# Optimization experiments

Measured on AMD Instinct MI355X. Metric: run time of the kernel, lower is better.

## Reference

```python
import jax, jax.numpy as jnp
import numpy as np
import math

C, N, D, D_CTX = 256, 512, 256, 256
K = 24
HOMEOSTASIS = 0.01
FEEDBACK = 0.3
B = 64


def setup_inputs() -> dict:
    key = jax.random.key(0)
    k1, k2, k3, k4, k5 = jax.random.split(key, 5)
    ff_scale = math.sqrt(2.0 / (D + N))
    ctx_scale = math.sqrt(2.0 / (D_CTX + N))
    pred_scale = math.sqrt(2.0 / (N + D))
    return {
        "x_input": jax.random.normal(k1, (B, D), dtype=jnp.float32),
        "x_context": jax.random.normal(k2, (B, D_CTX), dtype=jnp.float32),
        "W_ff": jax.random.normal(k3, (C, D, N), dtype=jnp.float32) * ff_scale,
        "W_ctx": jax.random.normal(k4, (C, D_CTX, N), dtype=jnp.float32) * ctx_scale,
        "W_pred": jax.random.normal(k5, (C, N, D), dtype=jnp.float32) * pred_scale,
        "bias": jnp.zeros((C, N), dtype=jnp.float32),
        "avg_activity": jnp.full((C, N), 0.05, dtype=jnp.float32),
    }


def _k_winners(drive, avg_activity, k):
    # homeostatic boosting: boost * homeostasis * 100
    boost = jnp.log1p(0.05 / (avg_activity + 1e-6))  # [C, N]
    boosted = drive + boost[None] * (HOMEOSTASIS * 100.0)
    topk_vals = jax.lax.top_k(boosted, k)[0]  # [B, C, k]
    threshold = jax.lax.stop_gradient(topk_vals[..., -1:])  # [B, C, 1]
    mask = (boosted >= threshold).astype(drive.dtype)
    activation = jax.nn.relu(drive) * mask
    activation = activation / (jnp.sum(activation, axis=-1, keepdims=True) + 1e-8) * k
    return activation


def reference(x_input, x_context, W_ff, W_ctx, W_pred, bias, avg_activity):
    # per-column feedforward + context drive: [B, C, N]
    ff_drive = jnp.einsum('bd,cdn->bcn', x_input, W_ff)
    ctx_drive = jnp.einsum('bd,cdn->bcn', x_context, W_ctx)
    drive = ff_drive + ctx_drive * FEEDBACK + bias[None]
    activations = _k_winners(drive, avg_activity, K)  # [B, C, N]
    predictions = jnp.einsum('bcn,cnd->bcd', activations, W_pred)  # [B, C, D]
    errors = x_input[:, None, :] - predictions  # [B, C, D]
    return activations, predictions, errors
```

## Files before the change

kernel.cpp:

```cpp
#include <hip/hip_runtime.h>
#include <math.h>

#define CC 256
#define NN 512
#define DD 256
#define BB 64
#define KK 24
#define WCAP 48

#define MAT_F (BB * NN)
#define SMEM_FLOATS (MAT_F + BB + BB + NN + BB + BB * WCAP * 2)
#define SMEM_BYTES (SMEM_FLOATS * 4)

__global__ void transpose_x_kernel(const float* __restrict__ x_in,
                                   const float* __restrict__ x_ctx,
                                   float* __restrict__ xT) {
  int idx = blockIdx.x * blockDim.x + threadIdx.x;
  int d = idx >> 6;
  int b = idx & 63;
  float v = (d < DD) ? x_in[b * DD + d] : 0.3f * x_ctx[b * DD + (d - DD)];
  xT[idx] = v;
}

__launch_bounds__(1024)
__global__ void cortical_main(const float* __restrict__ x_in,
                              const float* __restrict__ xT,
                              const float* __restrict__ W_ff,
                              const float* __restrict__ W_ctx,
                              const float* __restrict__ W_pred,
                              const float* __restrict__ bias,
                              const float* __restrict__ avg_act,
                              float* __restrict__ out_act,
                              float* __restrict__ out_pred,
                              float* __restrict__ out_err) {
  extern __shared__ float smem[];
  float* mat = smem;
  float* thr = smem + MAT_F;
  float* scl = thr + BB;
  float* boostS = scl + BB;
  int* wcnt = (int*)(boostS + NN);
  float* wlist = (float*)(wcnt + BB);

  const int c = blockIdx.x;
  const int t = threadIdx.x;
  const int lane = t & 63;
  const int wv = t >> 6;

  if (t < NN) boostS[t] = log1pf(0.05f / (avg_act[c * NN + t] + 1e-6f));
  __syncthreads();

  const int ng = t & 255;
  const int n0 = ng * 2;
  const int b0 = __builtin_amdgcn_readfirstlane((t >> 8) * 16);

  float acc[16][2];
#pragma unroll
  for (int i = 0; i < 16; ++i) { acc[i][0] = 0.f; acc[i][1] = 0.f; }

  const float* __restrict__ wf = W_ff + (size_t)c * DD * NN + n0;
  const float* __restrict__ wc = W_ctx + (size_t)c * DD * NN + n0;

#pragma unroll 4
  for (int d = 0; d < DD; ++d) {
    const float2 w = *reinterpret_cast<const float2*>(wf + (size_t)d * NN);
    const float* __restrict__ xp = xT + d * BB + b0;
#pragma unroll
    for (int i = 0; i < 16; ++i) {
      const float xv = xp[i];
      acc[i][0] = fmaf(xv, w.x, acc[i][0]);
      acc[i][1] = fmaf(xv, w.y, acc[i][1]);
    }
  }
#pragma unroll 4
  for (int d = 0; d < DD; ++d) {
    const float2 w = *reinterpret_cast<const float2*>(wc + (size_t)d * NN);
    const float* __restrict__ xp = xT + (DD + d) * BB + b0;
#pragma unroll
    for (int i = 0; i < 16; ++i) {
      const float xv = xp[i];
      acc[i][0] = fmaf(xv, w.x, acc[i][0]);
      acc[i][1] = fmaf(xv, w.y, acc[i][1]);
    }
  }

  const float2 bz = *reinterpret_cast<const float2*>(bias + (size_t)c * NN + n0);
  const float2 bo = *reinterpret_cast<const float2*>(boostS + n0);
#pragma unroll
  for (int i = 0; i < 16; ++i) {
    float d0v = acc[i][0] + bz.x;
    float d1v = acc[i][1] + bz.y;
    float2 m2;
    m2.x = d0v + bo.x;
    m2.y = d1v + bo.y;
    *reinterpret_cast<float2*>(mat + (size_t)(b0 + i) * NN + n0) = m2;
  }
  __syncthreads();

  for (int r = wv * 4; r < wv * 4 + 4; ++r) {
    float v[8];
#pragma unroll
    for (int j = 0; j < 8; ++j) v[j] = mat[r * NN + lane + 64 * j];
    float kth = 0.f;
    for (int it = 0; it < KK; ++it) {
      float m = v[0];
#pragma unroll
      for (int j = 1; j < 8; ++j) m = fmaxf(m, v[j]);
#pragma unroll
      for (int off = 1; off <= 32; off <<= 1) m = fmaxf(m, __shfl_xor(m, off));
      kth = m;
      bool mine = false;
#pragma unroll
      for (int j = 0; j < 8; ++j) mine = mine || (v[j] == m);
      unsigned long long msk = __ballot(mine);
      int first = __ffsll((unsigned long long)msk) - 1;
      if (lane == first) {
        bool done = false;
#pragma unroll
        for (int j = 0; j < 8; ++j) {
          bool cnd = (!done) && (v[j] == m);
          if (cnd) v[j] = -INFINITY;
          done = done || cnd;
        }
      }
    }
    if (lane == 0) thr[r] = kth;
  }
  __syncthreads();

  for (int r = wv * 4; r < wv * 4 + 4; ++r) {
    const float tb = thr[r];
    float raw[8];
    float s = 0.f;
#pragma unroll
    for (int j = 0; j < 8; ++j) {
      const int n = lane + 64 * j;
      const float bv = mat[r * NN + n];
      const float rw = (bv >= tb) ? fmaxf(bv - boostS[n], 0.f) : 0.f;
      raw[j] = rw;
      s += rw;
    }
#pragma unroll
    for (int off = 1; off <= 32; off <<= 1) s += __shfl_xor(s, off);
    const float sc = (float)KK / (s + 1e-8f);

    int base = 0;
#pragma unroll
    for (int j = 0; j < 8; ++j) {
      const int n = lane + 64 * j;
      const float a = raw[j] * sc;
      out_act[(size_t)r * (CC * NN) + (size_t)c * NN + n] = a;
      const bool win = a > 0.f;
      unsigned long long m = __ballot(win);
      int pos = base + __popcll(m & ((1ull << lane) - 1ull));
      if (win && pos < WCAP) {
        const int slot = (r * WCAP + pos) * 2;
        wlist[slot] = a;
        reinterpret_cast<int*>(wlist)[slot + 1] = n;
      }
      base += (int)__popcll(m);
    }
    if (lane == 0) wcnt[r] = (base < WCAP) ? base : WCAP;
  }
  __syncthreads();

  {
    const int dq = t & 63;
    const int d0 = dq * 4;
    const int grp = t >> 6;
    const float* __restrict__ wp = W_pred + (size_t)c * NN * DD;
    for (int bi = 0; bi < 4; ++bi) {
      const int b = grp * 4 + bi;
      const int cnt = wcnt[b];
      float4 p = make_float4(0.f, 0.f, 0.f, 0.f);
      float4 q = make_float4(0.f, 0.f, 0.f, 0.f);
      int i = 0;
      for (; i + 2 <= cnt; i += 2) {
        const int s0 = (b * WCAP + i) * 2;
        const int s1 = s0 + 2;
        const float a0 = wlist[s0];
        const int nn0 = reinterpret_cast<const int*>(wlist)[s0 + 1];
        const float a1 = wlist[s1];
        const int nn1 = reinterpret_cast<const int*>(wlist)[s1 + 1];
        const float4 w0 = *reinterpret_cast<const float4*>(wp + (size_t)nn0 * DD + d0);
        const float4 w1 = *reinterpret_cast<const float4*>(wp + (size_t)nn1 * DD + d0);
        p.x = fmaf(a0, w0.x, p.x); p.y = fmaf(a0, w0.y, p.y);
        p.z = fmaf(a0, w0.z, p.z); p.w = fmaf(a0, w0.w, p.w);
        q.x = fmaf(a1, w1.x, q.x); q.y = fmaf(a1, w1.y, q.y);
        q.z = fmaf(a1, w1.z, q.z); q.w = fmaf(a1, w1.w, q.w);
      }
      if (i < cnt) {
        const int s0 = (b * WCAP + i) * 2;
        const float a0 = wlist[s0];
        const int nn0 = reinterpret_cast<const int*>(wlist)[s0 + 1];
        const float4 w0 = *reinterpret_cast<const float4*>(wp + (size_t)nn0 * DD + d0);
        p.x = fmaf(a0, w0.x, p.x); p.y = fmaf(a0, w0.y, p.y);
        p.z = fmaf(a0, w0.z, p.z); p.w = fmaf(a0, w0.w, p.w);
      }
      float4 r4;
      r4.x = p.x + q.x; r4.y = p.y + q.y; r4.z = p.z + q.z; r4.w = p.w + q.w;
      const float4 xi = *reinterpret_cast<const float4*>(x_in + (size_t)b * DD + d0);
      float4 e4;
      e4.x = xi.x - r4.x; e4.y = xi.y - r4.y; e4.z = xi.z - r4.z; e4.w = xi.w - r4.w;
      *reinterpret_cast<float4*>(out_pred + (size_t)b * (CC * DD) + (size_t)c * DD + d0) = r4;
      *reinterpret_cast<float4*>(out_err + (size_t)b * (CC * DD) + (size_t)c * DD + d0) = e4;
    }
  }
}

extern "C" void kernel_launch(void* const* d_in, const int* in_sizes, int n_in,
                              void* d_out, int out_size, void* d_ws, size_t ws_size,
                              hipStream_t stream) {
  const float* x_in = (const float*)d_in[0];
  const float* x_ctx = (const float*)d_in[1];
  const float* W_ff = (const float*)d_in[2];
  const float* W_ctx = (const float*)d_in[3];
  const float* W_pred = (const float*)d_in[4];
  const float* bias = (const float*)d_in[5];
  const float* avg = (const float*)d_in[6];

  float* out = (float*)d_out;
  float* out_act = out;
  float* out_pred = out + (size_t)BB * CC * NN;
  float* out_err = out_pred + (size_t)BB * CC * DD;

  float* xT = (float*)d_ws;

  hipFuncSetAttribute((const void*)cortical_main,
                      hipFuncAttributeMaxDynamicSharedMemorySize, SMEM_BYTES);

  transpose_x_kernel<<<(2 * BB * DD) / 256, 256, 0, stream>>>(x_in, x_ctx, xT);
  cortical_main<<<CC, 1024, SMEM_BYTES, stream>>>(x_in, xT, W_ff, W_ctx, W_pred,
                                                  bias, avg, out_act, out_pred,
                                                  out_err);
}
```

Measured before the change: 218.9 us.

## Split fused kernel into drive GEMM and sparse top-k prediction kernels

Splits the single per-column kernel into a drive GEMM launched on twice as many blocks (each block covers half of N), writing the boosted drive to a workspace buffer, and a second kernel that reads it, does top-k, and computes the sparse prediction. The aim is to raise occupancy, since the old kernel needed about 140KB of LDS per block, and to remove the shared-memory staging and some barriers. In exchange it adds an extra global round trip of 32MB of drive data. The old fused kernel is kept as a fallback for when the workspace is too small.

Result: slower. 230.8 us (+5.4%).

```diff
diff --git a/kernel.cpp b/kernel.cpp
--- a/kernel.cpp
+++ b/kernel.cpp
@@ -7,10 +7,6 @@
 #define BB 64
 #define KK 24
 #define WCAP 48
-
-#define MAT_F (BB * NN)
-#define SMEM_FLOATS (MAT_F + BB + BB + NN + BB + BB * WCAP * 2)
-#define SMEM_BYTES (SMEM_FLOATS * 4)
 
 __global__ void transpose_x_kernel(const float* __restrict__ x_in,
                                    const float* __restrict__ x_ctx,
@@ -22,84 +18,92 @@
   xT[idx] = v;
 }
 
+__launch_bounds__(512)
+__global__ void drive_gemm(const float* __restrict__ xT,
+                           const float* __restrict__ W_ff,
+                           const float* __restrict__ W_ctx,
+                           const float* __restrict__ bias,
+                           const float* __restrict__ avg_act,
+                           float* __restrict__ driveB) {
+  const int c = blockIdx.x >> 1;
+  const int nh = blockIdx.x & 1;
+  const int t = threadIdx.x;
+  const int ng = t & 127;
+  const int n0 = nh * 256 + ng * 2;
+  const int b0 = __builtin_amdgcn_readfirstlane((t >> 7) * 16);
+
+  float2 acc[16];
+#pragma unroll
+  for (int i = 0; i < 16; ++i) { acc[i].x = 0.f; acc[i].y = 0.f; }
+
+  const float* __restrict__ wf = W_ff + (size_t)c * DD * NN + n0;
+  const float* __restrict__ wc = W_ctx + (size_t)c * DD * NN + n0;
+
+#pragma unroll 4
+  for (int d = 0; d < DD; ++d) {
+    const float2 w = *reinterpret_cast<const float2*>(wf + (size_t)d * NN);
+    const float* __restrict__ xp = xT + d * BB + b0;
+#pragma unroll
+    for (int i = 0; i < 16; ++i) {
+      const float xv = xp[i];
+      acc[i].x = fmaf(xv, w.x, acc[i].x);
+      acc[i].y = fmaf(xv, w.y, acc[i].y);
+    }
+  }
+#pragma unroll 4
+  for (int d = 0; d < DD; ++d) {
+    const float2 w = *reinterpret_cast<const float2*>(wc + (size_t)d * NN);
+    const float* __restrict__ xp = xT + (DD + d) * BB + b0;
+#pragma unroll
+    for (int i = 0; i < 16; ++i) {
+      const float xv = xp[i];
+      acc[i].x = fmaf(xv, w.x, acc[i].x);
+      acc[i].y = fmaf(xv, w.y, acc[i].y);
+    }
+  }
+
+  const float2 bz = *reinterpret_cast<const float2*>(bias + (size_t)c * NN + n0);
+  const float2 av = *reinterpret_cast<const float2*>(avg_act + (size_t)c * NN + n0);
+  float2 bo;
+  bo.x = log1pf(0.05f / (av.x + 1e-6f));
+  bo.y = log1pf(0.05f / (av.y + 1e-6f));
+
+#pragma unroll
+  for (int i = 0; i < 16; ++i) {
+    float2 m2;
+    m2.x = (acc[i].x + bz.x) + bo.x;
+    m2.y = (acc[i].y + bz.y) + bo.y;
+    *reinterpret_cast<float2*>(driveB + ((size_t)c * BB + (b0 + i)) * NN + n0) = m2;
+  }
+}
+
 __launch_bounds__(1024)
-__global__ void cortical_main(const float* __restrict__ x_in,
-                              const float* __restrict__ xT,
-                              const float* __restrict__ W_ff,
-                              const float* __restrict__ W_ctx,
-                              const float* __restrict__ W_pred,
-                              const float* __restrict__ bias,
-                              const float* __restrict__ avg_act,
-                              float* __restrict__ out_act,
-                              float* __restrict__ out_pred,
-                              float* __restrict__ out_err) {
-  extern __shared__ float smem[];
-  float* mat = smem;
-  float* thr = smem + MAT_F;
-  float* scl = thr + BB;
-  float* boostS = scl + BB;
-  int* wcnt = (int*)(boostS + NN);
-  float* wlist = (float*)(wcnt + BB);
+__global__ void sparse_pred(const float* __restrict__ x_in,
+                            const float* __restrict__ driveB,
+                            const float* __restrict__ W_pred,
+                            const float* __restrict__ avg_act,
+                            float* __restrict__ out_act,
+                            float* __restrict__ out_pred,
+                            float* __restrict__ out_err) {
+  __shared__ int wcnt[BB];
+  __shared__ float wlist[BB * WCAP * 2];
 
   const int c = blockIdx.x;
   const int t = threadIdx.x;
   const int lane = t & 63;
   const int wv = t >> 6;
 
-  if (t < NN) boostS[t] = log1pf(0.05f / (avg_act[c * NN + t] + 1e-6f));
-  __syncthreads();
-
-  const int ng = t & 255;
-  const int n0 = ng * 2;
-  const int b0 = __builtin_amdgcn_readfirstlane((t >> 8) * 16);
-
-  float acc[16][2];
-#pragma unroll
-  for (int i = 0; i < 16; ++i) { acc[i][0] = 0.f; acc[i][1] = 0.f; }
-
-  const float* __restrict__ wf = W_ff + (size_t)c * DD * NN + n0;
-  const float* __restrict__ wc = W_ctx + (size_t)c * DD * NN + n0;
-
-#pragma unroll 4
-  for (int d = 0; d < DD; ++d) {
-    const float2 w = *reinterpret_cast<const float2*>(wf + (size_t)d * NN);
-    const float* __restrict__ xp = xT + d * BB + b0;
-#pragma unroll
-    for (int i = 0; i < 16; ++i) {
-      const float xv = xp[i];
-      acc[i][0] = fmaf(xv, w.x, acc[i][0]);
-      acc[i][1] = fmaf(xv, w.y, acc[i][1]);
-    }
-  }
-#pragma unroll 4
-  for (int d = 0; d < DD; ++d) {
-    const float2 w = *reinterpret_cast<const float2*>(wc + (size_t)d * NN);
-    const float* __restrict__ xp = xT + (DD + d) * BB + b0;
-#pragma unroll
-    for (int i = 0; i < 16; ++i) {
-      const float xv = xp[i];
-      acc[i][0] = fmaf(xv, w.x, acc[i][0]);
-      acc[i][1] = fmaf(xv, w.y, acc[i][1]);
-    }
-  }
-
-  const float2 bz = *reinterpret_cast<const float2*>(bias + (size_t)c * NN + n0);
-  const float2 bo = *reinterpret_cast<const float2*>(boostS + n0);
-#pragma unroll
-  for (int i = 0; i < 16; ++i) {
-    float d0v = acc[i][0] + bz.x;
-    float d1v = acc[i][1] + bz.y;
-    float2 m2;
-    m2.x = d0v + bo.x;
-    m2.y = d1v + bo.y;
-    *reinterpret_cast<float2*>(mat + (size_t)(b0 + i) * NN + n0) = m2;
-  }
-  __syncthreads();
+  float bo[8];
+#pragma unroll
+  for (int j = 0; j < 8; ++j)
+    bo[j] = log1pf(0.05f / (avg_act[(size_t)c * NN + lane + 64 * j] + 1e-6f));
 
   for (int r = wv * 4; r < wv * 4 + 4; ++r) {
-    float v[8];
-#pragma unroll
-    for (int j = 0; j < 8; ++j) v[j] = mat[r * NN + lane + 64 * j];
+    const float* __restrict__ row = driveB + ((size_t)c * BB + r) * NN;
+    float o[8], v[8];
+#pragma unroll
+    for (int j = 0; j < 8; ++j) { o[j] = row[lane + 64 * j]; v[j] = o[j]; }
+
     float kth = 0.f;
     for (int it = 0; it < KK; ++it) {
       float m = v[0];
@@ -112,7 +116,7 @@
 #pragma unroll
       for (int j = 0; j < 8; ++j) mine = mine || (v[j] == m);
       unsigned long long msk = __ballot(mine);
-      int first = __ffsll((unsigned long long)msk) - 1;
+      int first = __ffsll(msk) - 1;
       if (lane == first) {
         bool done = false;
 #pragma unroll
@@ -123,19 +127,12 @@
         }
       }
     }
-    if (lane == 0) thr[r] = kth;
-  }
-  __syncthreads();
-
-  for (int r = wv * 4; r < wv * 4 + 4; ++r) {
-    const float tb = thr[r];
+
     float raw[8];
     float s = 0.f;
 #pragma unroll
     for (int j = 0; j < 8; ++j) {
-      const int n = lane + 64 * j;
-      const float bv = mat[r * NN + n];
-      const float rw = (bv >= tb) ? fmaxf(bv - boostS[n], 0.f) : 0.f;
+      const float rw = (o[j] >= kth) ? fmaxf(o[j] - bo[j], 0.f) : 0.f;
       raw[j] = rw;
       s += rw;
     }
@@ -207,6 +204,193 @@
   }
 }
 
+#define MAT_F (BB * NN)
+#define FSMEM_FLOATS (MAT_F + BB + BB + NN + BB + BB * WCAP * 2)
+#define FSMEM_BYTES (FSMEM_FLOATS * 4)
+
+__launch_bounds__(1024)
+__global__ void cortical_fused(const float* __restrict__ x_in,
+                               const float* __restrict__ xT,
+                               const float* __restrict__ W_ff,
+                               const float* __restrict__ W_ctx,
+                               const float* __restrict__ W_pred,
+                               const float* __restrict__ bias,
+                               const float* __restrict__ avg_act,
+                               float* __restrict__ out_act,
+                               float* __restrict__ out_pred,
+                               float* __restrict__ out_err) {
+  extern __shared__ float smem[];
+  float* mat = smem;
+  float* thr = smem + MAT_F;
+  float* scl = thr + BB;
+  float* boostS = scl + BB;
+  int* wcnt = (int*)(boostS + NN);
+  float* wlist = (float*)(wcnt + BB);
+
+  const int c = blockIdx.x;
+  const int t = threadIdx.x;
+  const int lane = t & 63;
+  const int wv = t >> 6;
+
+  if (t < NN) boostS[t] = log1pf(0.05f / (avg_act[c * NN + t] + 1e-6f));
+  __syncthreads();
+
+  const int ng = t & 255;
+  const int n0 = ng * 2;
+  const int b0 = __builtin_amdgcn_readfirstlane((t >> 8) * 16);
+
+  float acc[16][2];
+#pragma unroll
+  for (int i = 0; i < 16; ++i) { acc[i][0] = 0.f; acc[i][1] = 0.f; }
+
+  const float* __restrict__ wf = W_ff + (size_t)c * DD * NN + n0;
+  const float* __restrict__ wc = W_ctx + (size_t)c * DD * NN + n0;
+
+#pragma unroll 4
+  for (int d = 0; d < DD; ++d) {
+    const float2 w = *reinterpret_cast<const float2*>(wf + (size_t)d * NN);
+    const float* __restrict__ xp = xT + d * BB + b0;
+#pragma unroll
+    for (int i = 0; i < 16; ++i) {
+      const float xv = xp[i];
+      acc[i][0] = fmaf(xv, w.x, acc[i][0]);
+      acc[i][1] = fmaf(xv, w.y, acc[i][1]);
+    }
+  }
+#pragma unroll 4
+  for (int d = 0; d < DD; ++d) {
+    const float2 w = *reinterpret_cast<const float2*>(wc + (size_t)d * NN);
+    const float* __restrict__ xp = xT + (DD + d) * BB + b0;
+#pragma unroll
+    for (int i = 0; i < 16; ++i) {
+      const float xv = xp[i];
+      acc[i][0] = fmaf(xv, w.x, acc[i][0]);
+      acc[i][1] = fmaf(xv, w.y, acc[i][1]);
+    }
+  }
+
+  const float2 bz = *reinterpret_cast<const float2*>(bias + (size_t)c * NN + n0);
+  const float2 bo = *reinterpret_cast<const float2*>(boostS + n0);
+#pragma unroll
+  for (int i = 0; i < 16; ++i) {
+    float2 m2;
+    m2.x = (acc[i][0] + bz.x) + bo.x;
+    m2.y = (acc[i][1] + bz.y) + bo.y;
+    *reinterpret_cast<float2*>(mat + (size_t)(b0 + i) * NN + n0) = m2;
+  }
+  __syncthreads();
+
+  for (int r = wv * 4; r < wv * 4 + 4; ++r) {
+    float v[8];
+#pragma unroll
+    for (int j = 0; j < 8; ++j) v[j] = mat[r * NN + lane + 64 * j];
+    float kth = 0.f;
+    for (int it = 0; it < KK; ++it) {
+      float m = v[0];
+#pragma unroll
+      for (int j = 1; j < 8; ++j) m = fmaxf(m, v[j]);
+#pragma unroll
+      for (int off = 1; off <= 32; off <<= 1) m = fmaxf(m, __shfl_xor(m, off));
+      kth = m;
+      bool mine = false;
+#pragma unroll
+      for (int j = 0; j < 8; ++j) mine = mine || (v[j] == m);
+      unsigned long long msk = __ballot(mine);
+      int first = __ffsll(msk) - 1;
+      if (lane == first) {
+        bool done = false;
+#pragma unroll
+        for (int j = 0; j < 8; ++j) {
+          bool cnd = (!done) && (v[j] == m);
+          if (cnd) v[j] = -INFINITY;
+          done = done || cnd;
+        }
+      }
+    }
+    if (lane == 0) thr[r] = kth;
+  }
+  __syncthreads();
+
+  for (int r = wv * 4; r < wv * 4 + 4; ++r) {
+    const float tb = thr[r];
+    float raw[8];
+    float s = 0.f;
+#pragma unroll
+    for (int j = 0; j < 8; ++j) {
+      const int n = lane + 64 * j;
+      const float bv = mat[r * NN + n];
+      const float rw = (bv >= tb) ? fmaxf(bv - boostS[n], 0.f) : 0.f;
+      raw[j] = rw;
+      s += rw;
+    }
+#pragma unroll
+    for (int off = 1; off <= 32; off <<= 1) s += __shfl_xor(s, off);
+    const float sc = (float)KK / (s + 1e-8f);
+
+    int base = 0;
+#pragma unroll
+    for (int j = 0; j < 8; ++j) {
+      const int n = lane + 64 * j;
+      const float a = raw[j] * sc;
+      out_act[(size_t)r * (CC * NN) + (size_t)c * NN + n] = a;
+      const bool win = a > 0.f;
+      unsigned long long m = __ballot(win);
+      int pos = base + __popcll(m & ((1ull << lane) - 1ull));
+      if (win && pos < WCAP) {
+        const int slot = (r * WCAP + pos) * 2;
+        wlist[slot] = a;
+        reinterpret_cast<int*>(wlist)[slot + 1] = n;
+      }
+      base += (int)__popcll(m);
+    }
+    if (lane == 0) wcnt[r] = (base < WCAP) ? base : WCAP;
+  }
+  __syncthreads();
+
+  {
+    const int dq = t & 63;
+    const int d0 = dq * 4;
+    const int grp = t >> 6;
+    const float* __restrict__ wp = W_pred + (size_t)c * NN * DD;
+    for (int bi = 0; bi < 4; ++bi) {
+      const int b = grp * 4 + bi;
+      const int cnt = wcnt[b];
+      float4 p = make_float4(0.f, 0.f, 0.f, 0.f);
+      float4 q = make_float4(0.f, 0.f, 0.f, 0.f);
+      int i = 0;
+      for (; i + 2 <= cnt; i += 2) {
+        const int s0 = (b * WCAP + i) * 2;
+        const int s1 = s0 + 2;
+        const float a0 = wlist[s0];
+        const int nn0 = reinterpret_cast<const int*>(wlist)[s0 + 1];
+        const float a1 = wlist[s1];
+        const int nn1 = reinterpret_cast<const int*>(wlist)[s1 + 1];
+        const float4 w0 = *reinterpret_cast<const float4*>(wp + (size_t)nn0 * DD + d0);
+        const float4 w1 = *reinterpret_cast<const float4*>(wp + (size_t)nn1 * DD + d0);
+        p.x = fmaf(a0, w0.x, p.x); p.y = fmaf(a0, w0.y, p.y);
+        p.z = fmaf(a0, w0.z, p.z); p.w = fmaf(a0, w0.w, p.w);
+        q.x = fmaf(a1, w1.x, q.x); q.y = fmaf(a1, w1.y, q.y);
+        q.z = fmaf(a1, w1.z, q.z); q.w = fmaf(a1, w1.w, q.w);
+      }
+      if (i < cnt) {
+        const int s0 = (b * WCAP + i) * 2;
+        const float a0 = wlist[s0];
+        const int nn0 = reinterpret_cast<const int*>(wlist)[s0 + 1];
+        const float4 w0 = *reinterpret_cast<const float4*>(wp + (size_t)nn0 * DD + d0);
+        p.x = fmaf(a0, w0.x, p.x); p.y = fmaf(a0, w0.y, p.y);
+        p.z = fmaf(a0, w0.z, p.z); p.w = fmaf(a0, w0.w, p.w);
+      }
+      float4 r4;
+      r4.x = p.x + q.x; r4.y = p.y + q.y; r4.z = p.z + q.z; r4.w = p.w + q.w;
+      const float4 xi = *reinterpret_cast<const float4*>(x_in + (size_t)b * DD + d0);
+      float4 e4;
+      e4.x = xi.x - r4.x; e4.y = xi.y - r4.y; e4.z = xi.z - r4.z; e4.w = xi.w - r4.w;
+      *reinterpret_cast<float4*>(out_pred + (size_t)b * (CC * DD) + (size_t)c * DD + d0) = r4;
+      *reinterpret_cast<float4*>(out_err + (size_t)b * (CC * DD) + (size_t)c * DD + d0) = e4;
+    }
+  }
+}
+
 extern "C" void kernel_launch(void* const* d_in, const int* in_sizes, int n_in,
                               void* d_out, int out_size, void* d_ws, size_t ws_size,
                               hipStream_t stream) {
@@ -224,12 +408,21 @@
   float* out_err = out_pred + (size_t)BB * CC * DD;
 
   float* xT = (float*)d_ws;
-
-  hipFuncSetAttribute((const void*)cortical_main,
-                      hipFuncAttributeMaxDynamicSharedMemorySize, SMEM_BYTES);
+  float* driveB = xT + 2 * BB * DD;
+
+  const size_t need_bytes = (size_t)(2 * BB * DD + (size_t)CC * BB * NN) * 4;
 
   transpose_x_kernel<<<(2 * BB * DD) / 256, 256, 0, stream>>>(x_in, x_ctx, xT);
-  cortical_main<<<CC, 1024, SMEM_BYTES, stream>>>(x_in, xT, W_ff, W_ctx, W_pred,
-                                                  bias, avg, out_act, out_pred,
-                                                  out_err);
+
+  if (ws_size >= need_bytes) {
+    drive_gemm<<<2 * CC, 512, 0, stream>>>(xT, W_ff, W_ctx, bias, avg, driveB);
+    sparse_pred<<<CC, 1024, 0, stream>>>(x_in, driveB, W_pred, avg, out_act,
+                                         out_pred, out_err);
+  } else {
+    hipFuncSetAttribute((const void*)cortical_fused,
+                        hipFuncAttributeMaxDynamicSharedMemorySize, FSMEM_BYTES);
+    cortical_fused<<<CC, 1024, FSMEM_BYTES, stream>>>(x_in, xT, W_ff, W_ctx,
+                                                      W_pred, bias, avg, out_act,
+                                                      out_pred, out_err);
+  }
 }
```
